# Optimization experiments

Hardware: AMD Instinct MI355X
Metric: run time of the kernel (lower is better)

Reference implementation:

```python
import jax, jax.numpy as jnp
import numpy as np

DIM = 1024
N = 8192


def setup_inputs() -> dict:
    key = jax.random.key(0)
    k_x, k_w, k_b = jax.random.split(key, 3)
    inputs = jax.random.normal(k_x, (N, DIM), dtype=jnp.float32)
    # nn.Bilinear(dimension, dimension, 1): weight shape (1, d, d), bias shape (1,)
    bound = 1.0 / np.sqrt(DIM)
    W = jax.random.uniform(k_w, (DIM, DIM), jnp.float32, -bound, bound)
    b = jax.random.uniform(k_b, (1,), jnp.float32, -bound, bound)
    return {"inputs": inputs, "W": W, "b": b}


def reference(inputs, W, b):
    # out[i, j] = inputs[i] @ W @ inputs[j] + b  ==  (X @ W) @ X^T + b
    # Algebraically identical to repeat+nn.Bilinear, without the N^2*d blowup.
    xw = inputs @ W              # (N, d)
    out = xw @ inputs.T + b[0]   # (N, N)
    return out
```

## Files before the change

### kernel.cpp

```cpp
#include <hip/hip_runtime.h>
#include <hip/hip_bf16.h>

typedef __bf16 bf16;
typedef __bf16 bf16x8 __attribute__((ext_vector_type(8)));
typedef __bf16 bf16x4 __attribute__((ext_vector_type(4)));
typedef float  f32x4  __attribute__((ext_vector_type(4)));

#define GLD_LDS(g, l)                                                        \
  __builtin_amdgcn_global_load_lds(                                          \
      (const __attribute__((address_space(1))) void*)(g),                    \
      (__attribute__((address_space(3))) void*)(l), 16, 0, 0)

#define SB()    __builtin_amdgcn_s_barrier()
#define WVM(n)  asm volatile("s_waitcnt vmcnt(" #n ")" ::: "memory")
#define PRIO1() __builtin_amdgcn_s_setprio(1)
#define PRIO0() __builtin_amdgcn_s_setprio(0)

template <int EPI, int NP>
__global__ __launch_bounds__(512, 2)
void gemm256(const bf16* __restrict__ A, const bf16* __restrict__ B,
             bf16* __restrict__ Cb, float* __restrict__ Cf,
             const float* __restrict__ bias_p, int M) {
  constexpr int KP = 1024;
  constexpr int NT = KP / 64;
  extern __shared__ bf16 lds[];
  const int tid  = threadIdx.x;
  const int lane = tid & 63, wave = tid >> 6;
  const int wm = wave >> 2, wn = wave & 3;
  const int fr = lane & 15, fq = lane >> 4;
  const int xm = (fr & 7) << 4;
  const int kx0 = (fq * 16) ^ xm;
  const int kx1 = (fq * 16 + 64) ^ xm;

  const int nwg = gridDim.x;
  const int bid = blockIdx.x;
  constexpr int gx = NP >> 8;
  const int nTiles = (M >> 8) * gx;
  const int rounds = nTiles / nwg;

  const int srow = wave * 8 + (lane >> 3);
  const int scol = ((lane & 7) ^ (lane >> 3)) * 8;

  bf16* ldsA = lds + wave * 512;
  bf16* ldsB = lds + 32768 + wave * 512;
  const char* ldsc = (const char*)lds;
  const char* Ab0 = ldsc + wm * 16384 + fr * 128 + kx0;
  const char* Ab1 = ldsc + wm * 16384 + fr * 128 + kx1;
  const char* Bb0 = ldsc + 65536 + wn * 8192 + fr * 128 + kx0;
  const char* Bb1 = ldsc + 65536 + wn * 8192 + fr * 128 + kx1;

  const float bias = (EPI == 1) ? bias_p[0] : 0.0f;

#define STG2(p0, p1, trel, base, off)                                        \
  do {                                                                       \
    GLD_LDS((p0) + (trel) * 64, (base) + (off));                             \
    GLD_LDS((p1) + (trel) * 64, (base) + (off) + 4096);                      \
  } while (0)

#define LDA4(mg, kk, p)                                                      \
  do {                                                                       \
    _Pragma("unroll") for (int m_ = 0; m_ < 4; ++m_)                         \
      af[m_][kk] = *(const bf16x8*)(Ab##kk + (p) * 32768 +                   \
                                    ((mg) * 4 + m_) * 2048);                 \
  } while (0)

#define LDB2(np, kk, p)                                                      \
  do {                                                                       \
    _Pragma("unroll") for (int n_ = 0; n_ < 2; ++n_)                         \
      bg[(np) * 2 + n_][kk] = *(const bf16x8*)(Bb##kk + (p) * 32768 +        \
                                               ((np) * 2 + n_) * 2048);      \
  } while (0)

#define MM(mg, np)                                                           \
  do {                                                                       \
    _Pragma("unroll") for (int kk_ = 0; kk_ < 2; ++kk_)                      \
      _Pragma("unroll") for (int m_ = 0; m_ < 4; ++m_)                       \
        _Pragma("unroll") for (int n_ = 0; n_ < 2; ++n_)                     \
          acc[(mg) * 4 + m_][(np) * 2 + n_] =                                \
              __builtin_amdgcn_mfma_f32_16x16x32_bf16(                       \
                  af[m_][kk_], bg[(np) * 2 + n_][kk_],                       \
                  acc[(mg) * 4 + m_][(np) * 2 + n_], 0, 0, 0);               \
  } while (0)

#define PHASE(RDS, STAGE, MMC, GATE)                                         \
  do { RDS; STAGE; SB(); PRIO1(); MMC; PRIO0(); GATE; SB(); } while (0)

#define RD1 do { LDB2(0,0,0); LDA4(0,0,0); LDB2(0,1,0); LDA4(0,1,0); } while(0)
#define RD2 do { LDB2(1,0,0); LDB2(1,1,0); } while(0)
#define RD3 do { LDA4(1,0,0); LDA4(1,1,0); } while(0)
#define RD5 do { LDB2(0,0,1); LDA4(0,0,1); LDB2(0,1,1); LDA4(0,1,1); } while(0)
#define RD6 do { LDB2(1,0,1); LDB2(1,1,1); } while(0)
#define RD7 do { LDA4(1,0,1); LDA4(1,1,1); } while(0)

  auto mapTile = [&](int rd, int& tr, int& tc) {
    if (NP == 8192 && nwg == 256 && (M >> 8) == 32) {
      const int xcd = bid & 7, pos = bid >> 3;
      tr = (rd >> 1) * 16 + (xcd >> 1) * 4 + (pos >> 3);
      tc = (rd & 1) * 16 + (xcd & 1) * 8 + (pos & 7);
    } else {
      const int li = rd * nwg + bid;
      const int swz = (li & 7) * (nTiles >> 3) + (li >> 3);
      tr = li < nTiles ? swz / gx : 0; tc = li < nTiles ? swz % gx : 0;
    }
  };

  int tr, tc;
  mapTile(0, tr, tc);
  int row0 = tr << 8, col0 = tc << 8;

  const bf16* a0 = A + (size_t)(row0 + srow) * KP + scol;
  const bf16* a1 = a0 + (size_t)64 * KP;
  const bf16* a2 = a0 + (size_t)128 * KP;
  const bf16* a3 = a0 + (size_t)192 * KP;
  const bf16* b0 = B + (size_t)(col0 + srow) * KP + scol;
  const bf16* b1 = b0 + (size_t)64 * KP;
  const bf16* b2 = b0 + (size_t)128 * KP;
  const bf16* b3 = b0 + (size_t)192 * KP;

  STG2(a0, a1, 0, ldsA, 0);
  STG2(a2, a3, 0, ldsA, 8192);
  STG2(b0, b1, 0, ldsB, 0);
  STG2(b2, b3, 0, ldsB, 8192);
  STG2(a0, a1, 1, ldsA, 16384);

  for (int rd = 0; rd < rounds; ++rd) {
    if (rd == 0) { WVM(2); } else { WVM(32); }
    SB();

    f32x4  acc[8][4] = {};
    bf16x8 af[4][2];
    bf16x8 bg[4][2];

#pragma unroll 1
    for (int it = 0; it < NT / 2 - 1; ++it) {
      PHASE(RD1, STG2(a2, a3, 1, ldsA, 24576), MM(0, 0), );
      PHASE(RD2, STG2(b0, b1, 1, ldsB, 16384), MM(0, 1), );
      PHASE(RD3, STG2(b2, b3, 1, ldsB, 24576), MM(1, 0), );
      PHASE(   , STG2(a0, a1, 2, ldsA, 0),     MM(1, 1), WVM(2));
      PHASE(RD5, STG2(a2, a3, 2, ldsA, 8192),  MM(0, 0), );
      PHASE(RD6, STG2(b0, b1, 2, ldsB, 0),     MM(0, 1), );
      PHASE(RD7, STG2(b2, b3, 2, ldsB, 8192),  MM(1, 0), );
      PHASE(   , STG2(a0, a1, 3, ldsA, 16384), MM(1, 1), WVM(2));
      a0 += 128; a1 += 128; a2 += 128; a3 += 128;
      b0 += 128; b1 += 128; b2 += 128; b3 += 128;
    }

    const bool hn = (rd + 1 < rounds);
    int ntr, ntc;
    mapTile(rd + 1, ntr, ntc);
    const int nrow0 = ntr << 8, ncol0 = ntc << 8;
    const bf16* na0 = A + (size_t)(nrow0 + srow) * KP + scol;
    const bf16* na1 = na0 + (size_t)64 * KP;
    const bf16* na2 = na0 + (size_t)128 * KP;
    const bf16* na3 = na0 + (size_t)192 * KP;
    const bf16* nb0 = B + (size_t)(ncol0 + srow) * KP + scol;
    const bf16* nb1 = nb0 + (size_t)64 * KP;
    const bf16* nb2 = nb0 + (size_t)128 * KP;
    const bf16* nb3 = nb0 + (size_t)192 * KP;

    PHASE(RD1, STG2(a2, a3, 1, ldsA, 24576), MM(0, 0), );
    PHASE(RD2, STG2(b0, b1, 1, ldsB, 16384), MM(0, 1), );
    PHASE(RD3, STG2(b2, b3, 1, ldsB, 24576), MM(1, 0), );
    PHASE(   , if (hn) { STG2(na0, na1, 0, ldsA, 0); },    MM(1, 1),
           if (hn) { WVM(2); } else { WVM(0); });
    PHASE(RD5, if (hn) { STG2(na2, na3, 0, ldsA, 8192); }, MM(0, 0), );
    PHASE(RD6, if (hn) { STG2(nb0, nb1, 0, ldsB, 0); },    MM(0, 1), );
    PHASE(RD7, if (hn) { STG2(nb2, nb3, 0, ldsB, 8192); }, MM(1, 0), );
    PHASE(   , if (hn) { STG2(na0, na1, 1, ldsA, 16384); }, MM(1, 1),
           if (hn) { WVM(2); } else { WVM(0); });

    if (EPI == 1) {
      float* ldse = (float*)(ldsc + 98304);
#pragma unroll
      for (int q2 = 0; q2 < 8; ++q2) {
        const int h = q2 >> 2, q = q2 & 3;
        if (wm == h) {
#pragma unroll
          for (int mh = 0; mh < 2; ++mh)
#pragma unroll
            for (int n = 0; n < 4; ++n)
#pragma unroll
              for (int j = 0; j < 4; ++j) {
                const int rl = mh * 16 + fq * 4 + j;
                const int cl = (wn * 64 + n * 16 + fr) ^ (fq << 4);
                ldse[rl * 256 + cl] = acc[q * 2 + mh][n][j];
              }
        }
        SB();
#pragma unroll
        for (int i = 0; i < 4; ++i) {
          const int rl = i * 8 + wave;
          const int s = (rl >> 2) & 3;
          const f32x4 v =
              *(const f32x4*)&ldse[rl * 256 + ((lane * 4) ^ (s << 4))];
          f32x4 o;
          o[0] = v[0] + bias; o[1] = v[1] + bias;
          o[2] = v[2] + bias; o[3] = v[3] + bias;
          *(f32x4*)&Cf[(size_t)(row0 + h * 128 + q * 32 + rl) * NP + col0 +
                       lane * 4] = o;
        }
        SB();
      }
    } else {
#pragma unroll
      for (int m = 0; m < 8; ++m) {
#pragma unroll
        for (int n = 0; n < 4; ++n) {
          const int r = row0 + wm * 128 + m * 16 + fq * 4;
          const int c = col0 + wn * 64 + n * 16 + fr;
#pragma unroll
          for (int j = 0; j < 4; ++j)
            Cb[(size_t)(r + j) * NP + c] = (bf16)acc[m][n][j];
        }
      }
    }

    a0 = na0; a1 = na1; a2 = na2; a3 = na3;
    b0 = nb0; b1 = nb1; b2 = nb2; b3 = nb3;
    row0 = nrow0; col0 = ncol0;
  }
#undef STG2
#undef LDA4
#undef LDB2
#undef MM
#undef PHASE
#undef RD1
#undef RD2
#undef RD3
#undef RD5
#undef RD6
#undef RD7
}

__global__ void cvt_f32_bf16(const float* __restrict__ in, bf16* __restrict__ out,
                             int n4) {
  int i = blockIdx.x * blockDim.x + threadIdx.x;
  if (i >= n4) return;
  const float4 v = ((const float4*)in)[i];
  bf16x4 o;
  o[0] = (bf16)v.x; o[1] = (bf16)v.y; o[2] = (bf16)v.z; o[3] = (bf16)v.w;
  ((bf16x4*)out)[i] = o;
}

__global__ void transpose_cvt_w(const float* __restrict__ W, bf16* __restrict__ Wt) {
  __shared__ float s[32][33];
  const int tx = threadIdx.x & 31;
  const int ty = threadIdx.x >> 5;
  const int n0 = blockIdx.x * 32;
  const int k0 = blockIdx.y * 32;
#pragma unroll
  for (int p = 0; p < 4; ++p)
    s[ty + p * 8][tx] = W[(size_t)(k0 + ty + p * 8) * 1024 + n0 + tx];
  __syncthreads();
#pragma unroll
  for (int p = 0; p < 4; ++p)
    Wt[(size_t)(n0 + ty + p * 8) * 1024 + k0 + tx] = (bf16)s[tx][ty + p * 8];
}

extern "C" void kernel_launch(void* const* d_in, const int* in_sizes, int n_in,
                              void* d_out, int out_size, void* d_ws, size_t ws_size,
                              hipStream_t stream) {
  const float* X = (const float*)d_in[0];
  const float* W = (const float*)d_in[1];
  const float* b = (const float*)d_in[2];
  float* out = (float*)d_out;

  const int Nn = 8192, D = 1024;
  char* ws = (char*)d_ws;
  bf16* Xb  = (bf16*)(ws);
  bf16* XWb = (bf16*)(ws + (size_t)16 * 1024 * 1024);
  bf16* Wt  = (bf16*)(ws + (size_t)32 * 1024 * 1024);

  cvt_f32_bf16<<<(Nn * D / 4 + 255) / 256, 256, 0, stream>>>(X, Xb, Nn * D / 4);
  transpose_cvt_w<<<dim3(D / 32, D / 32), 256, 0, stream>>>(W, Wt);
  gemm256<0, 1024><<<128, 512, 131072, stream>>>(Xb, Wt, XWb, nullptr, nullptr,
                                                 Nn);
  gemm256<1, 8192><<<256, 512, 131072, stream>>>(XWb, Xb, nullptr, out, b, Nn);
}
```

Before: 194.6 us.

## Replace persistent multi-round GEMM with one-tile-per-block launch and merge prep kernels

The second GEMM no longer loops persistently over four tile rounds per block. It launches 1024 blocks, each computing one 256x256 tile, with the XCD-aware tile mapping derived from the block index. The tail no longer prefetches the next tile, so the epilogue of one tile can no longer overlap with loads for the next. The f32-to-bf16 conversion of X and the transpose/convert of W are fused into a single prep kernel to remove one launch. The trade-off is more block launches and more prologue/epilogue overhead per tile, in exchange for simpler control flow and hardware-managed scheduling.

```diff
diff --git a/kernel.cpp b/kernel.cpp
--- a/kernel.cpp
+++ b/kernel.cpp
@@ -32,11 +32,21 @@
   const int kx0 = (fq * 16) ^ xm;
   const int kx1 = (fq * 16 + 64) ^ xm;
 
-  const int nwg = gridDim.x;
   const int bid = blockIdx.x;
   constexpr int gx = NP >> 8;
-  const int nTiles = (M >> 8) * gx;
-  const int rounds = nTiles / nwg;
+
+  int tr, tc;
+  if (NP == 8192 && gridDim.x == 1024) {
+    const int round = bid >> 8, idx = bid & 255;
+    const int xcd = idx & 7, pos = idx >> 3;
+    tr = (round >> 1) * 16 + (xcd >> 1) * 4 + (pos >> 3);
+    tc = (round & 1) * 16 + (xcd & 1) * 8 + (pos & 7);
+  } else {
+    const int nTiles = (M >> 8) * gx;
+    const int swz = (bid & 7) * (nTiles >> 3) + (bid >> 3);
+    tr = swz / gx; tc = swz % gx;
+  }
+  const int row0 = tr << 8, col0 = tc << 8;
 
   const int srow = wave * 8 + (lane >> 3);
   const int scol = ((lane & 7) ^ (lane >> 3)) * 8;
@@ -91,22 +101,6 @@
 #define RD5 do { LDB2(0,0,1); LDA4(0,0,1); LDB2(0,1,1); LDA4(0,1,1); } while(0)
 #define RD6 do { LDB2(1,0,1); LDB2(1,1,1); } while(0)
 #define RD7 do { LDA4(1,0,1); LDA4(1,1,1); } while(0)
-
-  auto mapTile = [&](int rd, int& tr, int& tc) {
-    if (NP == 8192 && nwg == 256 && (M >> 8) == 32) {
-      const int xcd = bid & 7, pos = bid >> 3;
-      tr = (rd >> 1) * 16 + (xcd >> 1) * 4 + (pos >> 3);
-      tc = (rd & 1) * 16 + (xcd & 1) * 8 + (pos & 7);
-    } else {
-      const int li = rd * nwg + bid;
-      const int swz = (li & 7) * (nTiles >> 3) + (li >> 3);
-      tr = li < nTiles ? swz / gx : 0; tc = li < nTiles ? swz % gx : 0;
-    }
-  };
-
-  int tr, tc;
-  mapTile(0, tr, tc);
-  int row0 = tr << 8, col0 = tc << 8;
 
   const bf16* a0 = A + (size_t)(row0 + srow) * KP + scol;
   const bf16* a1 = a0 + (size_t)64 * KP;
@@ -122,102 +116,79 @@
   STG2(b0, b1, 0, ldsB, 0);
   STG2(b2, b3, 0, ldsB, 8192);
   STG2(a0, a1, 1, ldsA, 16384);
-
-  for (int rd = 0; rd < rounds; ++rd) {
-    if (rd == 0) { WVM(2); } else { WVM(32); }
-    SB();
-
-    f32x4  acc[8][4] = {};
-    bf16x8 af[4][2];
-    bf16x8 bg[4][2];
+  WVM(2); SB();
+
+  f32x4  acc[8][4] = {};
+  bf16x8 af[4][2];
+  bf16x8 bg[4][2];
 
 #pragma unroll 1
-    for (int it = 0; it < NT / 2 - 1; ++it) {
-      PHASE(RD1, STG2(a2, a3, 1, ldsA, 24576), MM(0, 0), );
-      PHASE(RD2, STG2(b0, b1, 1, ldsB, 16384), MM(0, 1), );
-      PHASE(RD3, STG2(b2, b3, 1, ldsB, 24576), MM(1, 0), );
-      PHASE(   , STG2(a0, a1, 2, ldsA, 0),     MM(1, 1), WVM(2));
-      PHASE(RD5, STG2(a2, a3, 2, ldsA, 8192),  MM(0, 0), );
-      PHASE(RD6, STG2(b0, b1, 2, ldsB, 0),     MM(0, 1), );
-      PHASE(RD7, STG2(b2, b3, 2, ldsB, 8192),  MM(1, 0), );
-      PHASE(   , STG2(a0, a1, 3, ldsA, 16384), MM(1, 1), WVM(2));
-      a0 += 128; a1 += 128; a2 += 128; a3 += 128;
-      b0 += 128; b1 += 128; b2 += 128; b3 += 128;
-    }
-
-    const bool hn = (rd + 1 < rounds);
-    int ntr, ntc;
-    mapTile(rd + 1, ntr, ntc);
-    const int nrow0 = ntr << 8, ncol0 = ntc << 8;
-    const bf16* na0 = A + (size_t)(nrow0 + srow) * KP + scol;
-    const bf16* na1 = na0 + (size_t)64 * KP;
-    const bf16* na2 = na0 + (size_t)128 * KP;
-    const bf16* na3 = na0 + (size_t)192 * KP;
-    const bf16* nb0 = B + (size_t)(ncol0 + srow) * KP + scol;
-    const bf16* nb1 = nb0 + (size_t)64 * KP;
-    const bf16* nb2 = nb0 + (size_t)128 * KP;
-    const bf16* nb3 = nb0 + (size_t)192 * KP;
-
+  for (int it = 0; it < NT / 2 - 1; ++it) {
     PHASE(RD1, STG2(a2, a3, 1, ldsA, 24576), MM(0, 0), );
     PHASE(RD2, STG2(b0, b1, 1, ldsB, 16384), MM(0, 1), );
     PHASE(RD3, STG2(b2, b3, 1, ldsB, 24576), MM(1, 0), );
-    PHASE(   , if (hn) { STG2(na0, na1, 0, ldsA, 0); },    MM(1, 1),
-           if (hn) { WVM(2); } else { WVM(0); });
-    PHASE(RD5, if (hn) { STG2(na2, na3, 0, ldsA, 8192); }, MM(0, 0), );
-    PHASE(RD6, if (hn) { STG2(nb0, nb1, 0, ldsB, 0); },    MM(0, 1), );
-    PHASE(RD7, if (hn) { STG2(nb2, nb3, 0, ldsB, 8192); }, MM(1, 0), );
-    PHASE(   , if (hn) { STG2(na0, na1, 1, ldsA, 16384); }, MM(1, 1),
-           if (hn) { WVM(2); } else { WVM(0); });
-
-    if (EPI == 1) {
-      float* ldse = (float*)(ldsc + 98304);
-#pragma unroll
-      for (int q2 = 0; q2 < 8; ++q2) {
-        const int h = q2 >> 2, q = q2 & 3;
-        if (wm == h) {
-#pragma unroll
-          for (int mh = 0; mh < 2; ++mh)
-#pragma unroll
-            for (int n = 0; n < 4; ++n)
-#pragma unroll
-              for (int j = 0; j < 4; ++j) {
-                const int rl = mh * 16 + fq * 4 + j;
-                const int cl = (wn * 64 + n * 16 + fr) ^ (fq << 4);
-                ldse[rl * 256 + cl] = acc[q * 2 + mh][n][j];
-              }
-        }
-        SB();
-#pragma unroll
-        for (int i = 0; i < 4; ++i) {
-          const int rl = i * 8 + wave;
-          const int s = (rl >> 2) & 3;
-          const f32x4 v =
-              *(const f32x4*)&ldse[rl * 256 + ((lane * 4) ^ (s << 4))];
-          f32x4 o;
-          o[0] = v[0] + bias; o[1] = v[1] + bias;
-          o[2] = v[2] + bias; o[3] = v[3] + bias;
-          *(f32x4*)&Cf[(size_t)(row0 + h * 128 + q * 32 + rl) * NP + col0 +
-                       lane * 4] = o;
-        }
-        SB();
+    PHASE(   , STG2(a0, a1, 2, ldsA, 0),     MM(1, 1), WVM(2));
+    PHASE(RD5, STG2(a2, a3, 2, ldsA, 8192),  MM(0, 0), );
+    PHASE(RD6, STG2(b0, b1, 2, ldsB, 0),     MM(0, 1), );
+    PHASE(RD7, STG2(b2, b3, 2, ldsB, 8192),  MM(1, 0), );
+    PHASE(   , STG2(a0, a1, 3, ldsA, 16384), MM(1, 1), WVM(2));
+    a0 += 128; a1 += 128; a2 += 128; a3 += 128;
+    b0 += 128; b1 += 128; b2 += 128; b3 += 128;
+  }
+
+  PHASE(RD1, STG2(a2, a3, 1, ldsA, 24576), MM(0, 0), );
+  PHASE(RD2, STG2(b0, b1, 1, ldsB, 16384), MM(0, 1), );
+  PHASE(RD3, STG2(b2, b3, 1, ldsB, 24576), MM(1, 0), );
+  PHASE(   ,                              , MM(1, 1), WVM(0));
+  PHASE(RD5,                              , MM(0, 0), );
+  PHASE(RD6,                              , MM(0, 1), );
+  PHASE(RD7,                              , MM(1, 0), );
+  PHASE(   ,                              , MM(1, 1), WVM(0));
+
+  if (EPI == 1) {
+    float* ldse = (float*)(ldsc + 98304);
+#pragma unroll
+    for (int q2 = 0; q2 < 8; ++q2) {
+      const int h = q2 >> 2, q = q2 & 3;
+      if (wm == h) {
+#pragma unroll
+        for (int mh = 0; mh < 2; ++mh)
+#pragma unroll
+          for (int n = 0; n < 4; ++n)
+#pragma unroll
+            for (int j = 0; j < 4; ++j) {
+              const int rl = mh * 16 + fq * 4 + j;
+              const int cl = (wn * 64 + n * 16 + fr) ^ (fq << 4);
+              ldse[rl * 256 + cl] = acc[q * 2 + mh][n][j];
+            }
       }
-    } else {
-#pragma unroll
-      for (int m = 0; m < 8; ++m) {
-#pragma unroll
-        for (int n = 0; n < 4; ++n) {
-          const int r = row0 + wm * 128 + m * 16 + fq * 4;
-          const int c = col0 + wn * 64 + n * 16 + fr;
-#pragma unroll
-          for (int j = 0; j < 4; ++j)
-            Cb[(size_t)(r + j) * NP + c] = (bf16)acc[m][n][j];
-        }
+      SB();
+#pragma unroll
+      for (int i = 0; i < 4; ++i) {
+        const int rl = i * 8 + wave;
+        const int s = (rl >> 2) & 3;
+        const f32x4 v =
+            *(const f32x4*)&ldse[rl * 256 + ((lane * 4) ^ (s << 4))];
+        f32x4 o;
+        o[0] = v[0] + bias; o[1] = v[1] + bias;
+        o[2] = v[2] + bias; o[3] = v[3] + bias;
+        *(f32x4*)&Cf[(size_t)(row0 + h * 128 + q * 32 + rl) * NP + col0 +
+                     lane * 4] = o;
+      }
+      SB();
+    }
+  } else {
+#pragma unroll
+    for (int m = 0; m < 8; ++m) {
+#pragma unroll
+      for (int n = 0; n < 4; ++n) {
+        const int r = row0 + wm * 128 + m * 16 + fq * 4;
+        const int c = col0 + wn * 64 + n * 16 + fr;
+#pragma unroll
+        for (int j = 0; j < 4; ++j)
+          Cb[(size_t)(r + j) * NP + c] = (bf16)acc[m][n][j];
       }
     }
-
-    a0 = na0; a1 = na1; a2 = na2; a3 = na3;
-    b0 = nb0; b1 = nb1; b2 = nb2; b3 = nb3;
-    row0 = nrow0; col0 = ncol0;
   }
 #undef STG2
 #undef LDA4
@@ -232,29 +203,30 @@
 #undef RD7
 }
 
-__global__ void cvt_f32_bf16(const float* __restrict__ in, bf16* __restrict__ out,
-                             int n4) {
-  int i = blockIdx.x * blockDim.x + threadIdx.x;
-  if (i >= n4) return;
-  const float4 v = ((const float4*)in)[i];
-  bf16x4 o;
-  o[0] = (bf16)v.x; o[1] = (bf16)v.y; o[2] = (bf16)v.z; o[3] = (bf16)v.w;
-  ((bf16x4*)out)[i] = o;
-}
-
-__global__ void transpose_cvt_w(const float* __restrict__ W, bf16* __restrict__ Wt) {
+__global__ void prep(const float* __restrict__ X, bf16* __restrict__ Xb,
+                     const float* __restrict__ W, bf16* __restrict__ Wt) {
   __shared__ float s[32][33];
-  const int tx = threadIdx.x & 31;
-  const int ty = threadIdx.x >> 5;
-  const int n0 = blockIdx.x * 32;
-  const int k0 = blockIdx.y * 32;
-#pragma unroll
-  for (int p = 0; p < 4; ++p)
-    s[ty + p * 8][tx] = W[(size_t)(k0 + ty + p * 8) * 1024 + n0 + tx];
-  __syncthreads();
-#pragma unroll
-  for (int p = 0; p < 4; ++p)
-    Wt[(size_t)(n0 + ty + p * 8) * 1024 + k0 + tx] = (bf16)s[tx][ty + p * 8];
+  const int bid = blockIdx.x;
+  if (bid < 8192) {
+    const int i = bid * 256 + threadIdx.x;
+    const float4 v = ((const float4*)X)[i];
+    bf16x4 o;
+    o[0] = (bf16)v.x; o[1] = (bf16)v.y; o[2] = (bf16)v.z; o[3] = (bf16)v.w;
+    ((bf16x4*)Xb)[i] = o;
+  } else {
+    const int b2 = bid - 8192;
+    const int tx = threadIdx.x & 31;
+    const int ty = threadIdx.x >> 5;
+    const int n0 = (b2 & 31) * 32;
+    const int k0 = (b2 >> 5) * 32;
+#pragma unroll
+    for (int p = 0; p < 4; ++p)
+      s[ty + p * 8][tx] = W[(size_t)(k0 + ty + p * 8) * 1024 + n0 + tx];
+    __syncthreads();
+#pragma unroll
+    for (int p = 0; p < 4; ++p)
+      Wt[(size_t)(n0 + ty + p * 8) * 1024 + k0 + tx] = (bf16)s[tx][ty + p * 8];
+  }
 }
 
 extern "C" void kernel_launch(void* const* d_in, const int* in_sizes, int n_in,
@@ -265,15 +237,14 @@
   const float* b = (const float*)d_in[2];
   float* out = (float*)d_out;
 
-  const int Nn = 8192, D = 1024;
+  const int Nn = 8192;
   char* ws = (char*)d_ws;
   bf16* Xb  = (bf16*)(ws);
   bf16* XWb = (bf16*)(ws + (size_t)16 * 1024 * 1024);
   bf16* Wt  = (bf16*)(ws + (size_t)32 * 1024 * 1024);
 
-  cvt_f32_bf16<<<(Nn * D / 4 + 255) / 256, 256, 0, stream>>>(X, Xb, Nn * D / 4);
-  transpose_cvt_w<<<dim3(D / 32, D / 32), 256, 0, stream>>>(W, Wt);
+  prep<<<9216, 256, 0, stream>>>(X, Xb, W, Wt);
   gemm256<0, 1024><<<128, 512, 131072, stream>>>(Xb, Wt, XWb, nullptr, nullptr,
                                                  Nn);
-  gemm256<1, 8192><<<256, 512, 131072, stream>>>(XWb, Xb, nullptr, out, b, Nn);
+  gemm256<1, 8192><<<1024, 512, 131072, stream>>>(XWb, Xb, nullptr, out, b, Nn);
 }
```

Measured after the change: 192.1 us. Within noise of the previous version (-1.3%).
